# Performance work log

Hardware: AMD Instinct MI355X
Metric: run time of the kernel (lower is better)

The kernel has to match this reference:

```python
import jax, jax.numpy as jnp
import numpy as np

B, F, D = 16384, 32, 64   # batch, n_continuous_features, input_dim
H = 2 * D                  # hidden = 2*input_dim per the d_hidden spec


def setup_inputs() -> dict:
    key = jax.random.key(0)
    ks = jax.random.split(key, 6)
    s1 = 1.0 / np.sqrt(D).astype(np.float32)
    s2 = 1.0 / np.sqrt(H).astype(np.float32)
    return {
        "X": jax.random.normal(ks[0], (B, F), jnp.float32),
        "r_": jax.random.normal(ks[1], (B, F, D), jnp.float32),
        # stacked per-feature weights (one tiny MLP per continuous column)
        "W1": jax.random.normal(ks[2], (F, D, H), jnp.float32) * s1,
        "b1": jax.random.normal(ks[3], (F, H), jnp.float32) * s1,
        "W2": jax.random.normal(ks[4], (F, H, 1), jnp.float32) * s2,
        "b2": jax.random.normal(ks[5], (F, 1), jnp.float32) * s2,
    }


def reference(X, r_, W1, b1, W2, b2):
    # Per-feature 2-layer MLP (Linear->relu->Linear->relu), batched over the
    # feature axis instead of the original Python loop over ModuleDict.
    h = jax.nn.relu(jnp.einsum('bfd,fdh->bfh', r_, W1) + b1)   # [B,F,H]
    y = jax.nn.relu(jnp.einsum('bfh,fho->bfo', h, W2) + b2)    # [B,F,1]
    x = X[..., None]                                           # [B,F,1] raw scalar per column
    # Original returns list of (x_col, mlp_out) pairs; we pack them as [B,F,2]
    # with [...,0]=x and [...,1]=mlp output (same values, dense layout).
    return jnp.concatenate([x, y], axis=-1)
```

## Files before the change

kernel.cpp:

```cpp
#include <hip/hip_runtime.h>
#include <hip/hip_bf16.h>
#include <stdint.h>

#define B_SZ 16384
#define F_SZ 32
#define D_SZ 64
#define H_SZ 128
#define RSTRIDE 72

typedef __attribute__((ext_vector_type(8))) short  short8;
typedef __attribute__((ext_vector_type(4))) float  float4v;
typedef __attribute__((ext_vector_type(4))) unsigned int uint4v;

__device__ __forceinline__ unsigned int pkbf(float lo, float hi) {
  unsigned int ulo = __builtin_bit_cast(unsigned int, lo) + 0x8000u;
  unsigned int uhi = __builtin_bit_cast(unsigned int, hi) + 0x8000u;
  return __builtin_amdgcn_perm(uhi, ulo, 0x07060302u);
}

__global__ __launch_bounds__(256) void ContMlp_prep(
    const float* __restrict__ W1, const float* __restrict__ b1,
    const float* __restrict__ W2, unsigned short* __restrict__ w1t,
    unsigned int* __restrict__ bw) {
  const int f  = blockIdx.x >> 2;
  const int hq = blockIdx.x & 3;
  const int h0 = hq * 32;
  const int t  = threadIdx.x;
  __shared__ float lds[D_SZ][33];
  const float* w1f = W1 + (size_t)f * (D_SZ * H_SZ);
#pragma unroll
  for (int i = 0; i < 8; ++i) {
    int idx = t + 256 * i;
    int d = idx >> 5, hh = idx & 31;
    lds[d][hh] = w1f[d * H_SZ + h0 + hh];
  }
  __syncthreads();
  unsigned short* o = w1t + (size_t)f * (H_SZ * D_SZ);
#pragma unroll
  for (int i = 0; i < 8; ++i) {
    int idx = t + 256 * i;
    int hh = idx >> 6, d = idx & 63;
    unsigned int u = __builtin_bit_cast(unsigned int, lds[d][hh]) + 0x8000u;
    o[(h0 + hh) * D_SZ + d] = (unsigned short)(u >> 16);
  }
  if (hq == 0 && t < H_SZ) {
    unsigned int ub = __builtin_bit_cast(unsigned int, b1[f * H_SZ + t]) + 0x8000u;
    unsigned int uw = __builtin_bit_cast(unsigned int, W2[f * H_SZ + t]) + 0x8000u;
    bw[f * H_SZ + t] = (ub & 0xFFFF0000u) | (uw >> 16);
  }
}

__device__ __forceinline__ void compute_sub(
    const float4v* c,
    const unsigned short* w1l, const unsigned int* bwl,
    float b2f, int col, int quad, float* store_ptr) {
  unsigned int p0 = pkbf(c[0].x, c[0].y), p1 = pkbf(c[0].z, c[0].w);
  unsigned int p2 = pkbf(c[1].x, c[1].y), p3 = pkbf(c[1].z, c[1].w);
  unsigned int p4 = pkbf(c[2].x, c[2].y), p5 = pkbf(c[2].z, c[2].w);
  unsigned int p6 = pkbf(c[3].x, c[3].y), p7 = pkbf(c[3].z, c[3].w);
  uint4v bq0 = {p0, p1, p2, p3};
  uint4v bq1 = {p4, p5, p6, p7};
  short8 bf0 = __builtin_bit_cast(short8, bq0);
  short8 bf1 = __builtin_bit_cast(short8, bq1);

  float ysum = 0.f;
#pragma unroll
  for (int t = 0; t < 8; ++t) {
    const unsigned short* wrow = w1l + (col + 16 * t) * RSTRIDE + quad * 8;
    short8 a0 = *(const short8*)(wrow);
    short8 a1 = *(const short8*)(wrow + 32);
    float4v acc = {0.f, 0.f, 0.f, 0.f};
    acc = __builtin_amdgcn_mfma_f32_16x16x32_bf16(a0, bf0, acc, 0, 0, 0);
    acc = __builtin_amdgcn_mfma_f32_16x16x32_bf16(a1, bf1, acc, 0, 0, 0);
    uint4v bwv = *(const uint4v*)(bwl + 16 * t + quad * 4);
#pragma unroll
    for (int r = 0; r < 4; ++r) {
      unsigned int u = bwv[r];
      float b1v = __builtin_bit_cast(float, u & 0xFFFF0000u);
      float w2v = __builtin_bit_cast(float, u << 16);
      ysum = fmaf(fmaxf(acc[r] + b1v, 0.f), w2v, ysum);
    }
  }
  ysum += __shfl_xor(ysum, 16, 64);
  ysum += __shfl_xor(ysum, 32, 64);
  float y = fmaxf(ysum + b2f, 0.f);
  if (quad == 0) *store_ptr = y;
}

__global__ __launch_bounds__(256, 4) void ContMlp_main(
    const float* __restrict__ r_,
    const unsigned short* __restrict__ w1t, const unsigned int* __restrict__ bw,
    const float* __restrict__ b2, float* __restrict__ ydst,
    int y_fmul, int y_rmul, int y_cadd) {
  const int f    = blockIdx.x & 31;
  const int tile = blockIdx.x >> 5;
  const int w    = threadIdx.x >> 6;
  const int l    = threadIdx.x & 63;
  const int col  = l & 15;
  const int quad = l >> 4;

  __shared__ unsigned short w1l[H_SZ * RSTRIDE];
  __shared__ unsigned int   bwl[H_SZ];

  {
    const uint4v* src = (const uint4v*)(w1t + (size_t)f * (H_SZ * D_SZ));
#pragma unroll
    for (int i = 0; i < 4; ++i) {
      int ci = threadIdx.x + 256 * i;
      int h = ci >> 3, dc = ci & 7;
      *(uint4v*)(w1l + h * RSTRIDE + dc * 8) = src[ci];
    }
    if (threadIdx.x < H_SZ) bwl[threadIdx.x] = bw[f * H_SZ + threadIdx.x];
  }
  __syncthreads();
  const float b2f = b2[f];

  const int row_w0 = tile * 512 + w * 128;
  const float* rbase = r_ + (size_t)(row_w0 + col) * (F_SZ * D_SZ)
                          + f * D_SZ + quad * 8;

  float4v buf[3][4];
#define LOADSUB(S, BI)                                                      \
  do {                                                                      \
    const float* p_ = rbase + (size_t)(S) * 16 * (F_SZ * D_SZ);             \
    buf[BI][0] = __builtin_nontemporal_load((const float4v*)(p_));          \
    buf[BI][1] = __builtin_nontemporal_load((const float4v*)(p_ + 4));      \
    buf[BI][2] = __builtin_nontemporal_load((const float4v*)(p_ + 32));     \
    buf[BI][3] = __builtin_nontemporal_load((const float4v*)(p_ + 36));     \
  } while (0)

  LOADSUB(0, 0);
  LOADSUB(1, 1);
#pragma unroll
  for (int s = 0; s < 8; ++s) {
    if (s + 2 < 8) LOADSUB(s + 2, (s + 2) % 3);
    float* yp = ydst + (size_t)f * y_fmul
                     + (size_t)(row_w0 + s * 16 + col) * y_rmul + y_cadd;
    compute_sub(buf[s % 3], w1l, bwl, b2f, col, quad, yp);
  }
#undef LOADSUB
}

__global__ __launch_bounds__(256) void ContMlp_combine(
    const float* __restrict__ X, const float* __restrict__ yws,
    float* __restrict__ out) {
  __shared__ float yl[F_SZ][33];
  const int r0 = blockIdx.x * 32;
  const int t = threadIdx.x;
#pragma unroll
  for (int i = 0; i < 4; ++i) {
    int idx = t + 256 * i;
    int f = idx >> 5, r = idx & 31;
    yl[f][r] = yws[(size_t)f * B_SZ + r0 + r];
  }
  __syncthreads();
#pragma unroll
  for (int i = 0; i < 4; ++i) {
    int idx = t + 256 * i;
    int r = idx >> 5, f = idx & 31;
    float2 o2 = make_float2(X[(size_t)(r0 + r) * F_SZ + f], yl[f][r]);
    *(float2*)(out + (size_t)(r0 + r) * (2 * F_SZ) + 2 * f) = o2;
  }
}

__global__ __launch_bounds__(256) void ContMlp_xwrite(
    const float* __restrict__ X, float* __restrict__ out) {
  int idx = blockIdx.x * 256 + threadIdx.x;
  int r = idx >> 5, f = idx & 31;
  out[(size_t)r * (2 * F_SZ) + 2 * f] = X[idx];
}

extern "C" void kernel_launch(void* const* d_in, const int* in_sizes, int n_in,
                              void* d_out, int out_size, void* d_ws, size_t ws_size,
                              hipStream_t stream) {
  const float* X  = (const float*)d_in[0];
  const float* r_ = (const float*)d_in[1];
  const float* W1 = (const float*)d_in[2];
  const float* b1 = (const float*)d_in[3];
  const float* W2 = (const float*)d_in[4];
  const float* b2 = (const float*)d_in[5];
  float* out = (float*)d_out;

  const size_t w1t_bytes = (size_t)F_SZ * H_SZ * D_SZ * 2;
  const size_t bw_off    = w1t_bytes;
  const size_t bw_bytes  = (size_t)F_SZ * H_SZ * 4;
  const size_t y_off     = bw_off + bw_bytes;
  const size_t y_bytes   = (size_t)B_SZ * F_SZ * 4;

  unsigned short* w1t = (unsigned short*)d_ws;
  unsigned int*   bw  = (unsigned int*)((char*)d_ws + bw_off);

  ContMlp_prep<<<F_SZ * 4, 256, 0, stream>>>(W1, b1, W2, w1t, bw);

  const bool pathA = ws_size >= y_off + y_bytes;
  if (pathA) {
    float* yws = (float*)((char*)d_ws + y_off);
    ContMlp_main<<<32 * F_SZ, 256, 0, stream>>>(r_, w1t, bw, b2, yws,
                                                B_SZ, 1, 0);
    ContMlp_combine<<<B_SZ / 32, 256, 0, stream>>>(X, yws, out);
  } else {
    ContMlp_main<<<32 * F_SZ, 256, 0, stream>>>(r_, w1t, bw, b2, out,
                                                2, 2 * F_SZ, 1);
    ContMlp_xwrite<<<(B_SZ * F_SZ) / 256, 256, 0, stream>>>(X, out);
  }
}
```

Before: 264.6 us.

## Pre-convert activations to bf16 in a separate pass before the MLP kernel

Adds a conversion kernel that rewrites the whole r_ tensor to bf16 in workspace, then runs a new main kernel that reads the bf16 copy with a one-step register prefetch. It also swaps the block-to-(feature, tile) mapping so consecutive blocks share a feature, and simplifies the f32 fallback by dropping the triple-buffered nontemporal loads and the occupancy hint. The extra pass reads all of r_ once and writes half that volume, which the main kernel then reads back. This likely adds memory traffic compared with converting inline.

```diff
diff --git a/kernel.cpp b/kernel.cpp
--- a/kernel.cpp
+++ b/kernel.cpp
@@ -16,6 +16,15 @@
   unsigned int ulo = __builtin_bit_cast(unsigned int, lo) + 0x8000u;
   unsigned int uhi = __builtin_bit_cast(unsigned int, hi) + 0x8000u;
   return __builtin_amdgcn_perm(uhi, ulo, 0x07060302u);
+}
+
+__global__ __launch_bounds__(256) void ContMlp_cvt(
+    const float* __restrict__ src, unsigned int* __restrict__ dst) {
+  size_t i = ((size_t)blockIdx.x * 256 + threadIdx.x) * 8;
+  float4v a = *(const float4v*)(src + i);
+  float4v b = *(const float4v*)(src + i + 4);
+  uint4v o = {pkbf(a.x, a.y), pkbf(a.z, a.w), pkbf(b.x, b.y), pkbf(b.z, b.w)};
+  *(uint4v*)(dst + i / 2) = o;
 }
 
 __global__ __launch_bounds__(256) void ContMlp_prep(
@@ -51,18 +60,9 @@
 }
 
 __device__ __forceinline__ void compute_sub(
-    const float4v* c,
+    short8 bf0, short8 bf1,
     const unsigned short* w1l, const unsigned int* bwl,
     float b2f, int col, int quad, float* store_ptr) {
-  unsigned int p0 = pkbf(c[0].x, c[0].y), p1 = pkbf(c[0].z, c[0].w);
-  unsigned int p2 = pkbf(c[1].x, c[1].y), p3 = pkbf(c[1].z, c[1].w);
-  unsigned int p4 = pkbf(c[2].x, c[2].y), p5 = pkbf(c[2].z, c[2].w);
-  unsigned int p6 = pkbf(c[3].x, c[3].y), p7 = pkbf(c[3].z, c[3].w);
-  uint4v bq0 = {p0, p1, p2, p3};
-  uint4v bq1 = {p4, p5, p6, p7};
-  short8 bf0 = __builtin_bit_cast(short8, bq0);
-  short8 bf1 = __builtin_bit_cast(short8, bq1);
-
   float ysum = 0.f;
 #pragma unroll
   for (int t = 0; t < 8; ++t) {
@@ -87,13 +87,61 @@
   if (quad == 0) *store_ptr = y;
 }
 
-__global__ __launch_bounds__(256, 4) void ContMlp_main(
+__global__ __launch_bounds__(256) void ContMlp_main_bf(
+    const unsigned short* __restrict__ rb,
+    const unsigned short* __restrict__ w1t, const unsigned int* __restrict__ bw,
+    const float* __restrict__ b2, float* __restrict__ ydst,
+    int y_fmul, int y_rmul, int y_cadd) {
+  const int f    = blockIdx.x >> 5;
+  const int tile = blockIdx.x & 31;
+  const int w    = threadIdx.x >> 6;
+  const int l    = threadIdx.x & 63;
+  const int col  = l & 15;
+  const int quad = l >> 4;
+
+  __shared__ unsigned short w1l[H_SZ * RSTRIDE];
+  __shared__ unsigned int   bwl[H_SZ];
+  {
+    const uint4v* src = (const uint4v*)(w1t + (size_t)f * (H_SZ * D_SZ));
+#pragma unroll
+    for (int i = 0; i < 4; ++i) {
+      int ci = threadIdx.x + 256 * i;
+      int h = ci >> 3, dc = ci & 7;
+      *(uint4v*)(w1l + h * RSTRIDE + dc * 8) = src[ci];
+    }
+    if (threadIdx.x < H_SZ) bwl[threadIdx.x] = bw[f * H_SZ + threadIdx.x];
+  }
+  __syncthreads();
+  const float b2f = b2[f];
+
+  const int row_w0 = tile * 512 + w * 128;
+  const unsigned short* bp = rb + (size_t)(row_w0 + col) * (F_SZ * D_SZ)
+                                + f * D_SZ + quad * 8;
+
+  short8 c0 = *(const short8*)(bp);
+  short8 c1 = *(const short8*)(bp + 32);
+#pragma unroll 1
+  for (int s = 0; s < 8; ++s) {
+    short8 n0, n1;
+    if (s < 7) {
+      const unsigned short* np = bp + (size_t)(s + 1) * 16 * (F_SZ * D_SZ);
+      n0 = *(const short8*)(np);
+      n1 = *(const short8*)(np + 32);
+    }
+    float* yp = ydst + (size_t)f * y_fmul
+                     + (size_t)(row_w0 + s * 16 + col) * y_rmul + y_cadd;
+    compute_sub(c0, c1, w1l, bwl, b2f, col, quad, yp);
+    c0 = n0; c1 = n1;
+  }
+}
+
+__global__ __launch_bounds__(256) void ContMlp_main_f32(
     const float* __restrict__ r_,
     const unsigned short* __restrict__ w1t, const unsigned int* __restrict__ bw,
     const float* __restrict__ b2, float* __restrict__ ydst,
     int y_fmul, int y_rmul, int y_cadd) {
-  const int f    = blockIdx.x & 31;
-  const int tile = blockIdx.x >> 5;
+  const int f    = blockIdx.x >> 5;
+  const int tile = blockIdx.x & 31;
   const int w    = threadIdx.x >> 6;
   const int l    = threadIdx.x & 63;
   const int col  = l & 15;
@@ -101,7 +149,6 @@
 
   __shared__ unsigned short w1l[H_SZ * RSTRIDE];
   __shared__ unsigned int   bwl[H_SZ];
-
   {
     const uint4v* src = (const uint4v*)(w1t + (size_t)f * (H_SZ * D_SZ));
 #pragma unroll
@@ -118,27 +165,20 @@
   const int row_w0 = tile * 512 + w * 128;
   const float* rbase = r_ + (size_t)(row_w0 + col) * (F_SZ * D_SZ)
                           + f * D_SZ + quad * 8;
-
-  float4v buf[3][4];
-#define LOADSUB(S, BI)                                                      \
-  do {                                                                      \
-    const float* p_ = rbase + (size_t)(S) * 16 * (F_SZ * D_SZ);             \
-    buf[BI][0] = __builtin_nontemporal_load((const float4v*)(p_));          \
-    buf[BI][1] = __builtin_nontemporal_load((const float4v*)(p_ + 4));      \
-    buf[BI][2] = __builtin_nontemporal_load((const float4v*)(p_ + 32));     \
-    buf[BI][3] = __builtin_nontemporal_load((const float4v*)(p_ + 36));     \
-  } while (0)
-
-  LOADSUB(0, 0);
-  LOADSUB(1, 1);
-#pragma unroll
+#pragma unroll 1
   for (int s = 0; s < 8; ++s) {
-    if (s + 2 < 8) LOADSUB(s + 2, (s + 2) % 3);
+    const float* p_ = rbase + (size_t)s * 16 * (F_SZ * D_SZ);
+    float4v r0 = *(const float4v*)(p_);
+    float4v r1 = *(const float4v*)(p_ + 4);
+    float4v r2 = *(const float4v*)(p_ + 32);
+    float4v r3 = *(const float4v*)(p_ + 36);
+    uint4v bq0 = {pkbf(r0.x, r0.y), pkbf(r0.z, r0.w), pkbf(r1.x, r1.y), pkbf(r1.z, r1.w)};
+    uint4v bq1 = {pkbf(r2.x, r2.y), pkbf(r2.z, r2.w), pkbf(r3.x, r3.y), pkbf(r3.z, r3.w)};
     float* yp = ydst + (size_t)f * y_fmul
                      + (size_t)(row_w0 + s * 16 + col) * y_rmul + y_cadd;
-    compute_sub(buf[s % 3], w1l, bwl, b2f, col, quad, yp);
-  }
-#undef LOADSUB
+    compute_sub(__builtin_bit_cast(short8, bq0), __builtin_bit_cast(short8, bq1),
+                w1l, bwl, b2f, col, quad, yp);
+  }
 }
 
 __global__ __launch_bounds__(256) void ContMlp_combine(
@@ -186,21 +226,33 @@
   const size_t bw_bytes  = (size_t)F_SZ * H_SZ * 4;
   const size_t y_off     = bw_off + bw_bytes;
   const size_t y_bytes   = (size_t)B_SZ * F_SZ * 4;
+  const size_t rb_off    = (y_off + y_bytes + 255) & ~(size_t)255;
+  const size_t rb_bytes  = (size_t)B_SZ * F_SZ * D_SZ * 2;
 
   unsigned short* w1t = (unsigned short*)d_ws;
   unsigned int*   bw  = (unsigned int*)((char*)d_ws + bw_off);
 
   ContMlp_prep<<<F_SZ * 4, 256, 0, stream>>>(W1, b1, W2, w1t, bw);
 
-  const bool pathA = ws_size >= y_off + y_bytes;
-  if (pathA) {
+  const bool haveY  = ws_size >= y_off + y_bytes;
+  const bool haveRb = ws_size >= rb_off + rb_bytes;
+
+  if (haveRb) {
+    unsigned short* rb = (unsigned short*)((char*)d_ws + rb_off);
     float* yws = (float*)((char*)d_ws + y_off);
-    ContMlp_main<<<32 * F_SZ, 256, 0, stream>>>(r_, w1t, bw, b2, yws,
-                                                B_SZ, 1, 0);
+    const size_t nElem = (size_t)B_SZ * F_SZ * D_SZ;
+    ContMlp_cvt<<<(unsigned)(nElem / (256 * 8)), 256, 0, stream>>>(r_, (unsigned int*)rb);
+    ContMlp_main_bf<<<32 * F_SZ, 256, 0, stream>>>(rb, w1t, bw, b2, yws,
+                                                   B_SZ, 1, 0);
+    ContMlp_combine<<<B_SZ / 32, 256, 0, stream>>>(X, yws, out);
+  } else if (haveY) {
+    float* yws = (float*)((char*)d_ws + y_off);
+    ContMlp_main_f32<<<32 * F_SZ, 256, 0, stream>>>(r_, w1t, bw, b2, yws,
+                                                    B_SZ, 1, 0);
     ContMlp_combine<<<B_SZ / 32, 256, 0, stream>>>(X, yws, out);
   } else {
-    ContMlp_main<<<32 * F_SZ, 256, 0, stream>>>(r_, w1t, bw, b2, out,
-                                                2, 2 * F_SZ, 1);
+    ContMlp_main_f32<<<32 * F_SZ, 256, 0, stream>>>(r_, w1t, bw, b2, out,
+                                                    2, 2 * F_SZ, 1);
     ContMlp_xwrite<<<(B_SZ * F_SZ) / 256, 256, 0, stream>>>(X, out);
   }
 }
```

After: 230.3 us. 13.0% less time.

## Stage r_ tiles via direct global-to-LDS loads instead of register prefetch

Applied to the files above, without the earlier changes.

Replaces the triple-buffered nontemporal register prefetch of r_ with per-wave `global_load_lds` transfers into a new LDS buffer. Each sub-tile is loaded, waited on with a full vmcnt wait, read back as float4 from LDS, then fed to the MFMAs. Outputs are buffered in registers and stored together at the end. The goal is to free vector registers and raise occupancy, since the launch-bounds occupancy hint is dropped. In exchange, software prefetch overlap within a wave is lost, and each block now uses extra LDS.

```diff
diff --git a/kernel.cpp b/kernel.cpp
--- a/kernel.cpp
+++ b/kernel.cpp
@@ -1,5 +1,4 @@
 #include <hip/hip_runtime.h>
-#include <hip/hip_bf16.h>
 #include <stdint.h>
 
 #define B_SZ 16384
@@ -50,44 +49,7 @@
   }
 }
 
-__device__ __forceinline__ void compute_sub(
-    const float4v* c,
-    const unsigned short* w1l, const unsigned int* bwl,
-    float b2f, int col, int quad, float* store_ptr) {
-  unsigned int p0 = pkbf(c[0].x, c[0].y), p1 = pkbf(c[0].z, c[0].w);
-  unsigned int p2 = pkbf(c[1].x, c[1].y), p3 = pkbf(c[1].z, c[1].w);
-  unsigned int p4 = pkbf(c[2].x, c[2].y), p5 = pkbf(c[2].z, c[2].w);
-  unsigned int p6 = pkbf(c[3].x, c[3].y), p7 = pkbf(c[3].z, c[3].w);
-  uint4v bq0 = {p0, p1, p2, p3};
-  uint4v bq1 = {p4, p5, p6, p7};
-  short8 bf0 = __builtin_bit_cast(short8, bq0);
-  short8 bf1 = __builtin_bit_cast(short8, bq1);
-
-  float ysum = 0.f;
-#pragma unroll
-  for (int t = 0; t < 8; ++t) {
-    const unsigned short* wrow = w1l + (col + 16 * t) * RSTRIDE + quad * 8;
-    short8 a0 = *(const short8*)(wrow);
-    short8 a1 = *(const short8*)(wrow + 32);
-    float4v acc = {0.f, 0.f, 0.f, 0.f};
-    acc = __builtin_amdgcn_mfma_f32_16x16x32_bf16(a0, bf0, acc, 0, 0, 0);
-    acc = __builtin_amdgcn_mfma_f32_16x16x32_bf16(a1, bf1, acc, 0, 0, 0);
-    uint4v bwv = *(const uint4v*)(bwl + 16 * t + quad * 4);
-#pragma unroll
-    for (int r = 0; r < 4; ++r) {
-      unsigned int u = bwv[r];
-      float b1v = __builtin_bit_cast(float, u & 0xFFFF0000u);
-      float w2v = __builtin_bit_cast(float, u << 16);
-      ysum = fmaf(fmaxf(acc[r] + b1v, 0.f), w2v, ysum);
-    }
-  }
-  ysum += __shfl_xor(ysum, 16, 64);
-  ysum += __shfl_xor(ysum, 32, 64);
-  float y = fmaxf(ysum + b2f, 0.f);
-  if (quad == 0) *store_ptr = y;
-}
-
-__global__ __launch_bounds__(256, 4) void ContMlp_main(
+__global__ __launch_bounds__(256) void ContMlp_main(
     const float* __restrict__ r_,
     const unsigned short* __restrict__ w1t, const unsigned int* __restrict__ bw,
     const float* __restrict__ b2, float* __restrict__ ydst,
@@ -101,6 +63,7 @@
 
   __shared__ unsigned short w1l[H_SZ * RSTRIDE];
   __shared__ unsigned int   bwl[H_SZ];
+  __shared__ float          rbuf[4][1024];
 
   {
     const uint4v* src = (const uint4v*)(w1t + (size_t)f * (H_SZ * D_SZ));
@@ -116,29 +79,65 @@
   const float b2f = b2[f];
 
   const int row_w0 = tile * 512 + w * 128;
-  const float* rbase = r_ + (size_t)(row_w0 + col) * (F_SZ * D_SZ)
-                          + f * D_SZ + quad * 8;
-
-  float4v buf[3][4];
-#define LOADSUB(S, BI)                                                      \
-  do {                                                                      \
-    const float* p_ = rbase + (size_t)(S) * 16 * (F_SZ * D_SZ);             \
-    buf[BI][0] = __builtin_nontemporal_load((const float4v*)(p_));          \
-    buf[BI][1] = __builtin_nontemporal_load((const float4v*)(p_ + 4));      \
-    buf[BI][2] = __builtin_nontemporal_load((const float4v*)(p_ + 32));     \
-    buf[BI][3] = __builtin_nontemporal_load((const float4v*)(p_ + 36));     \
-  } while (0)
-
-  LOADSUB(0, 0);
-  LOADSUB(1, 1);
-#pragma unroll
+  const float* gl = r_ + (size_t)(row_w0 + col) * (F_SZ * D_SZ)
+                       + f * D_SZ + quad * 4;
+  float* rb = &rbuf[w][0];
+  float yv[8];
+
+#pragma unroll 1
   for (int s = 0; s < 8; ++s) {
-    if (s + 2 < 8) LOADSUB(s + 2, (s + 2) % 3);
-    float* yp = ydst + (size_t)f * y_fmul
-                     + (size_t)(row_w0 + s * 16 + col) * y_rmul + y_cadd;
-    compute_sub(buf[s % 3], w1l, bwl, b2f, col, quad, yp);
-  }
-#undef LOADSUB
+    const float* gs = gl + (size_t)s * 16 * (F_SZ * D_SZ);
+#pragma unroll
+    for (int i = 0; i < 4; ++i) {
+      __builtin_amdgcn_global_load_lds(
+          (const __attribute__((address_space(1))) void*)(gs + i * 16),
+          (__attribute__((address_space(3))) void*)(rb + i * 256),
+          16, 0, 0);
+    }
+    __builtin_amdgcn_s_waitcnt(0x0F70);
+
+    float4v f0 = *(const float4v*)(rb + (quad * 2) * 64 + col * 4);
+    float4v f1 = *(const float4v*)(rb + (quad * 2 + 1) * 64 + col * 4);
+    float4v f2 = *(const float4v*)(rb + (8 + quad * 2) * 64 + col * 4);
+    float4v f3 = *(const float4v*)(rb + (9 + quad * 2) * 64 + col * 4);
+    uint4v bq0 = {pkbf(f0.x, f0.y), pkbf(f0.z, f0.w),
+                  pkbf(f1.x, f1.y), pkbf(f1.z, f1.w)};
+    uint4v bq1 = {pkbf(f2.x, f2.y), pkbf(f2.z, f2.w),
+                  pkbf(f3.x, f3.y), pkbf(f3.z, f3.w)};
+    short8 bf0 = __builtin_bit_cast(short8, bq0);
+    short8 bf1 = __builtin_bit_cast(short8, bq1);
+
+    float ysum = 0.f;
+#pragma unroll
+    for (int t = 0; t < 8; ++t) {
+      const unsigned short* wrow = w1l + (col + 16 * t) * RSTRIDE + quad * 8;
+      short8 a0 = *(const short8*)(wrow);
+      short8 a1 = *(const short8*)(wrow + 32);
+      float4v acc = {0.f, 0.f, 0.f, 0.f};
+      acc = __builtin_amdgcn_mfma_f32_16x16x32_bf16(a0, bf0, acc, 0, 0, 0);
+      acc = __builtin_amdgcn_mfma_f32_16x16x32_bf16(a1, bf1, acc, 0, 0, 0);
+      uint4v bwv = *(const uint4v*)(bwl + 16 * t + quad * 4);
+#pragma unroll
+      for (int r = 0; r < 4; ++r) {
+        unsigned int u = bwv[r];
+        float b1v = __builtin_bit_cast(float, u & 0xFFFF0000u);
+        float w2v = __builtin_bit_cast(float, u << 16);
+        ysum = fmaf(fmaxf(acc[r] + b1v, 0.f), w2v, ysum);
+      }
+    }
+    ysum += __shfl_xor(ysum, 16, 64);
+    ysum += __shfl_xor(ysum, 32, 64);
+    yv[s] = fmaxf(ysum + b2f, 0.f);
+  }
+
+  if (quad == 0) {
+#pragma unroll
+    for (int s = 0; s < 8; ++s) {
+      float* yp = ydst + (size_t)f * y_fmul
+                       + (size_t)(row_w0 + s * 16 + col) * y_rmul + y_cadd;
+      *yp = yv[s];
+    }
+  }
 }
 
 __global__ __launch_bounds__(256) void ContMlp_combine(
@@ -192,8 +191,7 @@
 
   ContMlp_prep<<<F_SZ * 4, 256, 0, stream>>>(W1, b1, W2, w1t, bw);
 
-  const bool pathA = ws_size >= y_off + y_bytes;
-  if (pathA) {
+  if (ws_size >= y_off + y_bytes) {
     float* yws = (float*)((char*)d_ws + y_off);
     ContMlp_main<<<32 * F_SZ, 256, 0, stream>>>(r_, w1t, bw, b2, yws,
                                                 B_SZ, 1, 0);
```

Measured after the change: 213.7 us (median of 2 runs). 19.2% less time.
